# Kernel optimization log

Hardware: AMD Instinct MI355X
Metric: run time of the kernel (lower is better)

## Reference

```python
import jax, jax.numpy as jnp
import numpy as np

# SLAYER neuron / simulation parameters (from network.yaml)
THETA = 10.0      # spike threshold
TAU_SR = 10.0     # SRM (psp) kernel time constant
TAU_REF = 1.0     # refractory kernel time constant
SCALE_REF = 2.0   # refractory scale (kernel = -scaleRef*theta*alpha(t))
TS = 1.0          # simulation step (ms)
TK = 100          # FIR truncation length for the psp kernel (tauSr=10 -> fully decayed)

B, NIN, NHID, NOUT, T = 32, 2312, 512, 10, 350

# discrete refractory kernel ref[n] = C_REF * n * D_REF**n  (alpha shape)
D_REF = float(np.exp(-TS / TAU_REF))
C_REF = float(-SCALE_REF * THETA * np.e * TS / TAU_REF)


def srm_kernel():
    # eps(t) = (t/tauSr) * exp(1 - t/tauSr), peak value 1 at t = tauSr
    t = jnp.arange(TK, dtype=jnp.float32) * TS
    return (t / TAU_SR) * jnp.exp(1.0 - t / TAU_SR)


def psp(x):
    """Causal FIR filter along time. x: [B, C, T] -> [B, C, T]."""
    b, c, t = x.shape
    k = srm_kernel()[::-1].reshape(1, 1, TK)  # lax.conv correlates, so flip
    xp = jnp.pad(x.reshape(b * c, 1, t), ((0, 0), (0, 0), (TK - 1, 0)))
    y = jax.lax.conv_general_dilated(xp, k, (1,), 'VALID')
    return y.reshape(b, c, t)


def dense(W, x):
    # 1x1 conv over channels, applied at every time step
    return jnp.einsum('oi,bit->bot', W, x)


@jax.custom_vjp
def spike_fn(u):
    return (u >= THETA).astype(u.dtype)

def _spike_fwd(u):
    return spike_fn(u), u

def _spike_bwd(u, g):
    # SLAYER surrogate gradient: rho(u) = scaleRho * exp(-|u - theta| / tauRho)
    return (g * jnp.exp(-jnp.abs(u - THETA) / 1.0),)

spike_fn.defvjp(_spike_fwd, _spike_bwd)


def spike_layer(u_in):
    """Threshold-and-refractory spike dynamics via a 2-state IIR realization of
    the alpha refractory kernel. u_in: [B, C, T] -> spikes [B, C, T]."""
    uT = jnp.moveaxis(u_in, -1, 0)  # [T, B, C]
    zero = jnp.zeros(uT.shape[1:], uT.dtype)

    def step(carry, u_t):
        a, b = carry  # a = conv(spikes, D^n), b = conv(spikes, n*D^n)
        u = u_t + C_REF * b          # membrane = psp drive + refractory
        s = spike_fn(u)
        a_new = D_REF * a + s
        b_new = D_REF * b + D_REF * a
        return (a_new, b_new), s

    _, sT = jax.lax.scan(step, (zero, zero), uT)
    return jnp.moveaxis(sT, 0, -1)


def setup_inputs() -> dict:
    key = jax.random.key(0)
    k1, k2, k3 = jax.random.split(key, 3)
    spikeInput = (jax.random.uniform(k1, (B, NIN, T)) < 0.05).astype(jnp.float32)
    W1 = jax.random.normal(k2, (NHID, NIN), dtype=jnp.float32) * 0.05
    W2 = jax.random.normal(k3, (NOUT, NHID), dtype=jnp.float32) * 0.05
    return {"spikeInput": spikeInput, "W1": W1, "W2": W2}


def reference(spikeInput, W1, W2):
    s1 = spike_layer(dense(W1, psp(spikeInput)))
    s2 = spike_layer(dense(W2, psp(s1)))
    return s2
```

## Files before the change

kernel.cpp:

```cpp
#include <hip/hip_runtime.h>
#include <stdint.h>

#define B_SZ   32
#define NIN    2312
#define NHID   512
#define NOUT   10
#define T_SZ   350
#define NW32   73
#define NW64   8
#define NHALF  256
#define NROW   2313

#define DS_D   0.9048374180359595
#define CS_D   0.2718281828459045
#define D100_D 4.5399929762484854e-05
#define DREF_F 0.36787944117144233f
#define CREF_F -54.36563656918091f

#define NCHUNK 7
#define CLEN   50
#define NPF    10

__global__ __launch_bounds__(384) void k12(const float* __restrict__ x,
                                           const float* __restrict__ W1,
                                           uint32_t* __restrict__ bits1,
                                           float* __restrict__ W1s) {
    __shared__ float lds[32 * T_SZ];
    const int bid = blockIdx.x;
    const int tid = threadIdx.x;
    if (bid < NW32 * B_SZ) {
        const int w = bid % NW32;
        const int b = bid / NW32;
        const int rows = (NIN - (w << 5) < 32) ? (NIN - (w << 5)) : 32;
        const float* base = x + ((size_t)(b * NIN + (w << 5))) * T_SZ;
        const int nf4 = (rows * T_SZ) >> 2;
        for (int f = tid; f < nf4; f += 384)
            ((float4*)lds)[f] = ((const float4*)base)[f];
        __syncthreads();
        if (tid < T_SZ) {
            uint32_t bits = 0;
            for (int j = 0; j < rows; ++j)
                bits |= (lds[j * T_SZ + tid] > 0.5f) ? (1u << j) : 0u;
            bits1[(size_t)(b * T_SZ + tid) * NW32 + w] = bits;
        }
    } else if (bid < NW32 * B_SZ + NW32 * 16) {
        float (*tile)[33] = (float (*)[33])lds;
        const int bb = bid - NW32 * B_SZ;
        const int i0 = (bb % NW32) * 32, o0 = (bb / NW32) * 32;
        const int tx = tid & 31, ty = tid >> 5;
#pragma unroll
        for (int r = 0; r < 3; ++r) {
            int row = ty + 12 * r;
            if (row < 32) {
                int o = o0 + row, i = i0 + tx;
                if (i < NIN) tile[row][tx] = W1[(size_t)o * NIN + i];
            }
        }
        __syncthreads();
#pragma unroll
        for (int r = 0; r < 3; ++r) {
            int row = ty + 12 * r;
            if (row < 32) {
                int i = i0 + row, o = o0 + tx;
                if (i < NIN)
                    W1s[((size_t)(o >> 8) * NROW + i) * NHALF + (o & 255)] = tile[tx][row];
            }
        }
    } else {
        if (tid < NHALF) {
            W1s[((size_t)0 * NROW + NIN) * NHALF + tid] = 0.0f;
            W1s[((size_t)1 * NROW + NIN) * NHALF + tid] = 0.0f;
        }
    }
}

__global__ __launch_bounds__(256) void k3_dense1(const uint32_t* __restrict__ bits1,
                                                 const float* __restrict__ W1s,
                                                 float* __restrict__ z1ct) {
    __shared__ uint32_t words[128];
    __shared__ uint16_t pfx[80];
    __shared__ uint16_t idxbuf[NIN + 16];
    __shared__ float red[3][NHALF];
    __shared__ float fin[NHALF];

    const int bt = blockIdx.x;
    const int h = blockIdx.y;
    const int tid = threadIdx.x;
    const int wv = tid >> 6, lane = tid & 63;

    if (tid < 128) words[tid] = (tid < NW32) ? bits1[(size_t)bt * NW32 + tid] : 0u;
    __syncthreads();

    if (wv == 0) {
        uint32_t w0 = words[lane];
        uint32_t w1 = words[lane + 64];
        int p0 = __popc(w0), p1 = __popc(w1);
        int s0 = p0, s1 = p1;
#pragma unroll
        for (int off = 1; off < 64; off <<= 1) {
            int u0 = __shfl_up(s0, off);
            int u1 = __shfl_up(s1, off);
            if (lane >= off) { s0 += u0; s1 += u1; }
        }
        int tot0 = __shfl(s0, 63);
        pfx[lane] = (uint16_t)(s0 - p0);
        if (lane < 9) pfx[lane + 64] = (uint16_t)(tot0 + s1 - p1);
        if (lane == 8) pfx[73] = (uint16_t)(tot0 + s1);
    }
    __syncthreads();

    const int ntot = pfx[73];
    const int npad = (ntot + 15) & ~15;
    if (tid < NW32) {
        uint32_t m = words[tid];
        int p = pfx[tid];
        while (m) {
            int j = __builtin_ctz(m);
            m &= m - 1;
            idxbuf[p++] = (uint16_t)((tid << 5) + j);
        }
    }
    if (tid >= 240) {
        int k = tid - 240;
        if (ntot + k < npad) idxbuf[ntot + k] = (uint16_t)NIN;
    }
    __syncthreads();

    const float* Wh = W1s + (size_t)h * NROW * NHALF;
    float4 acc = make_float4(0.f, 0.f, 0.f, 0.f);
    for (int r = wv; r < npad; r += 16) {
        int i0 = idxbuf[r], i1 = idxbuf[r + 4], i2 = idxbuf[r + 8], i3 = idxbuf[r + 12];
        float4 v0 = ((const float4*)(Wh + (size_t)i0 * NHALF))[lane];
        float4 v1 = ((const float4*)(Wh + (size_t)i1 * NHALF))[lane];
        float4 v2 = ((const float4*)(Wh + (size_t)i2 * NHALF))[lane];
        float4 v3 = ((const float4*)(Wh + (size_t)i3 * NHALF))[lane];
        acc.x += v0.x; acc.y += v0.y; acc.z += v0.z; acc.w += v0.w;
        acc.x += v1.x; acc.y += v1.y; acc.z += v1.z; acc.w += v1.w;
        acc.x += v2.x; acc.y += v2.y; acc.z += v2.z; acc.w += v2.w;
        acc.x += v3.x; acc.y += v3.y; acc.z += v3.z; acc.w += v3.w;
    }
    if (wv > 0) ((float4*)red[wv - 1])[lane] = acc;
    __syncthreads();
    if (wv == 0) {
        float4 a1 = ((float4*)red[0])[lane];
        float4 a2 = ((float4*)red[1])[lane];
        float4 a3 = ((float4*)red[2])[lane];
        acc.x = ((acc.x + a1.x) + a2.x) + a3.x;
        acc.y = ((acc.y + a1.y) + a2.y) + a3.y;
        acc.z = ((acc.z + a1.z) + a2.z) + a3.z;
        acc.w = ((acc.w + a1.w) + a2.w) + a3.w;
        ((float4*)fin)[lane] = acc;
    }
    __syncthreads();
    const int och = (h << 8) + tid;
    const int oc = och >> 6, l6 = och & 63;
    const int b = bt / T_SZ, t = bt - b * T_SZ;
    z1ct[((size_t)(b * NW64 + oc) * T_SZ + t) * 64 + l6] = fin[tid];
}

__global__ __launch_bounds__(512) void k45(const float* __restrict__ z1ct,
                                           const float* __restrict__ W2,
                                           float* __restrict__ z2ct) {
    __shared__ float W2s[NHID * NOUT];
    __shared__ uint64_t sw[CLEN][NW64];
    const int tid = threadIdx.x;
    const int wv = tid >> 6, lane = tid & 63;
    const int b = blockIdx.x / NCHUNK;
    const int ck = blockIdx.x % NCHUNK;
    const int tstart = ck * CLEN;
    const int tend = tstart + CLEN;
    const int t0 = (tstart >= 100) ? tstart - 100 : 0;

    for (int k = tid; k < NHID * NOUT; k += 512) {
        int c = k / NOUT, o = k - c * NOUT;
        W2s[k] = W2[(size_t)o * NHID + c];
    }

    const float* base = z1ct + (size_t)(b * NW64 + wv) * T_SZ * 64 + lane;
    double A = 0.0, Bs = 0.0, A2 = 0.0, Bs2 = 0.0;
    float ra = 0.0f, rb = 0.0f;
    const double TAIL = D100_D * CS_D;
    float xb[NPF], xdb[NPF];
#pragma unroll
    for (int i = 0; i < NPF; ++i) {
        int t = t0 + i;
        xb[i] = base[(size_t)t * 64];
        int td = t - 100;
        xdb[i] = (td >= 0) ? base[(size_t)td * 64] : 0.0f;
    }
    for (int tb = t0; tb < tend; tb += NPF) {
#pragma unroll
        for (int i = 0; i < NPF; ++i) {
            const int t = tb + i;
            float x = xb[i], xd = xdb[i];
            const int tn = t + NPF;
            xb[i] = (tn < T_SZ) ? base[(size_t)tn * 64] : 0.0f;
            const int td = tn - 100;
            xdb[i] = (td >= 0) ? base[(size_t)td * 64] : 0.0f;
            Bs = DS_D * Bs + DS_D * A;
            A = DS_D * A + (double)x;
            Bs2 = DS_D * Bs2 + DS_D * A2;
            A2 = DS_D * A2 + (double)xd;
            double y = CS_D * Bs - TAIL * (Bs2 + 100.0 * A2);
            float u = (float)y + CREF_F * rb;
            float s = (u >= 10.0f) ? 1.0f : 0.0f;
            float ran = DREF_F * ra + s;
            float rbn = DREF_F * rb + DREF_F * ra;
            ra = ran; rb = rbn;
            uint64_t mball = __ballot(s != 0.0f);
            if (t >= tstart && lane == 0) sw[t - tstart][wv] = mball;
        }
    }
    __syncthreads();

    if (tid < CLEN * NOUT) {
        const int tr = tid / NOUT;
        const int o = tid - tr * NOUT;
        const int t = tstart + tr;
        float acc = 0.f;
#pragma unroll
        for (int w2 = 0; w2 < NW64; ++w2) {
            uint64_t m = sw[tr][w2];
            while (m) {
                int j = __builtin_ctzll(m);
                m &= m - 1;
                acc += W2s[((w2 << 6) + j) * NOUT + o];
            }
        }
        const int bo = b * NOUT + o;
        z2ct[((size_t)(bo >> 6) * T_SZ + t) * 64 + (bo & 63)] = acc;
    }
}

__global__ __launch_bounds__(64) void k6_fir_scan2(const float* __restrict__ z2ct,
                                                   float* __restrict__ out) {
    const int lane = threadIdx.x;
    const int g = blockIdx.x / NCHUNK;
    const int ck = blockIdx.x % NCHUNK;
    const int tstart = ck * CLEN;
    const int tend = tstart + CLEN;
    const int t0 = (tstart >= 100) ? tstart - 100 : 0;
    const int bo = (g << 6) + lane;
    const float* base = z2ct + (size_t)g * T_SZ * 64 + lane;
    float* op = out + (size_t)bo * T_SZ;
    double A = 0.0, Bs = 0.0, A2 = 0.0, Bs2 = 0.0;
    float ra = 0.0f, rb = 0.0f;
    const double TAIL = D100_D * CS_D;
    float xb[NPF], xdb[NPF];
#pragma unroll
    for (int i = 0; i < NPF; ++i) {
        int t = t0 + i;
        xb[i] = base[(size_t)t * 64];
        int td = t - 100;
        xdb[i] = (td >= 0) ? base[(size_t)td * 64] : 0.0f;
    }
    for (int tb = t0; tb < tend; tb += NPF) {
#pragma unroll
        for (int i = 0; i < NPF; ++i) {
            const int t = tb + i;
            float x = xb[i], xd = xdb[i];
            const int tn = t + NPF;
            xb[i] = (tn < T_SZ) ? base[(size_t)tn * 64] : 0.0f;
            const int td = tn - 100;
            xdb[i] = (td >= 0) ? base[(size_t)td * 64] : 0.0f;
            Bs = DS_D * Bs + DS_D * A;
            A = DS_D * A + (double)x;
            Bs2 = DS_D * Bs2 + DS_D * A2;
            A2 = DS_D * A2 + (double)xd;
            double y = CS_D * Bs - TAIL * (Bs2 + 100.0 * A2);
            float u = (float)y + CREF_F * rb;
            float s = (u >= 10.0f) ? 1.0f : 0.0f;
            float ran = DREF_F * ra + s;
            float rbn = DREF_F * rb + DREF_F * ra;
            ra = ran; rb = rbn;
            if (t >= tstart) op[t] = s;
        }
    }
}

extern "C" void kernel_launch(void* const* d_in, const int* in_sizes, int n_in,
                              void* d_out, int out_size, void* d_ws, size_t ws_size,
                              hipStream_t stream) {
    const float* spikeInput = (const float*)d_in[0];
    const float* W1 = (const float*)d_in[1];
    const float* W2 = (const float*)d_in[2];
    float* out = (float*)d_out;

    char* ws = (char*)d_ws;
    float* W1s = (float*)(ws + 0);
    uint32_t* bits1 = (uint32_t*)(ws + 4737024);
    float* z1ct = (float*)(ws + 8007424);
    float* z2ct = (float*)(ws + 4737024);

    k12<<<NW32 * B_SZ + NW32 * 16 + 1, 384, 0, stream>>>(spikeInput, W1, bits1, W1s);
    k3_dense1<<<dim3(B_SZ * T_SZ, 2), 256, 0, stream>>>(bits1, W1s, z1ct);
    k45<<<B_SZ * NCHUNK, 512, 0, stream>>>(z1ct, W2, z2ct);
    k6_fir_scan2<<<5 * NCHUNK, 64, 0, stream>>>(z2ct, out);
}
```

Baseline: 316.4 us.

## Batch 32 time-columns per block in sparse dense1 to reuse W1 rows

The sparse dense1 kernel now handles 32 (batch,time) columns per block instead of one. It builds the union of active input rows plus a per-row 32-bit column mask. Each W1 row is then loaded once and added into every column whose mask bit is set, using wave-uniform branches. This is meant to cut repeated global/L2 reads of W1 rows that are shared across columns. In exchange it uses 32 accumulators per thread, more LDS, bit-transpose work, branchy accumulation and a much smaller grid.

Result: slower. 694.8 us (+119.6%).

```diff
diff --git a/kernel.cpp b/kernel.cpp
--- a/kernel.cpp
+++ b/kernel.cpp
@@ -20,6 +20,9 @@
 #define NCHUNK 7
 #define CLEN   50
 #define NPF    10
+
+#define GCOL   32
+#define NGRP   350
 
 __global__ __launch_bounds__(384) void k12(const float* __restrict__ x,
                                            const float* __restrict__ W1,
@@ -77,23 +80,45 @@
 __global__ __launch_bounds__(256) void k3_dense1(const uint32_t* __restrict__ bits1,
                                                  const float* __restrict__ W1s,
                                                  float* __restrict__ z1ct) {
-    __shared__ uint32_t words[128];
+    __shared__ uint32_t colw[GCOL * NW32];
+    __shared__ uint32_t orw[128];
+    __shared__ uint32_t rowmask[GCOL * NW32];
     __shared__ uint16_t pfx[80];
-    __shared__ uint16_t idxbuf[NIN + 16];
-    __shared__ float red[3][NHALF];
-    __shared__ float fin[NHALF];
-
-    const int bt = blockIdx.x;
+    __shared__ uint16_t idxbuf[NIN + 8];
+    __shared__ float red[GCOL][NHALF];
+
+    const int bt0 = blockIdx.x * GCOL;
     const int h = blockIdx.y;
     const int tid = threadIdx.x;
-    const int wv = tid >> 6, lane = tid & 63;
-
-    if (tid < 128) words[tid] = (tid < NW32) ? bits1[(size_t)bt * NW32 + tid] : 0u;
+    const int lane = tid & 63;
+    const int wv = tid >> 6;
+    const int g = tid >> 7;
+    const int l = tid & 127;
+
+    const uint32_t* bsrc = bits1 + (size_t)bt0 * NW32;
+    if (tid < 128) orw[tid] = 0;
+    for (int k = tid; k < GCOL * NW32; k += 256) colw[k] = bsrc[k];
+    __syncthreads();
+
+    if (tid < NW32) {
+        uint32_t o = 0;
+#pragma unroll
+        for (int c = 0; c < GCOL; ++c) o |= colw[c * NW32 + tid];
+        orw[tid] = o;
+    }
+    for (int k = tid; k < GCOL * NW32; k += 256) {
+        const int w = k >> 5, j = k & 31;
+        uint32_t m = 0;
+#pragma unroll
+        for (int c = 0; c < GCOL; ++c)
+            m |= ((colw[c * NW32 + w] >> j) & 1u) << c;
+        rowmask[k] = m;
+    }
     __syncthreads();
 
     if (wv == 0) {
-        uint32_t w0 = words[lane];
-        uint32_t w1 = words[lane + 64];
+        uint32_t w0 = orw[lane];
+        uint32_t w1 = orw[lane + 64];
         int p0 = __popc(w0), p1 = __popc(w1);
         int s0 = p0, s1 = p1;
 #pragma unroll
@@ -108,11 +133,10 @@
         if (lane == 8) pfx[73] = (uint16_t)(tot0 + s1);
     }
     __syncthreads();
-
     const int ntot = pfx[73];
-    const int npad = (ntot + 15) & ~15;
+    const int npad = (ntot + 7) & ~7;
     if (tid < NW32) {
-        uint32_t m = words[tid];
+        uint32_t m = orw[tid];
         int p = pfx[tid];
         while (m) {
             int j = __builtin_ctz(m);
@@ -120,42 +144,75 @@
             idxbuf[p++] = (uint16_t)((tid << 5) + j);
         }
     }
-    if (tid >= 240) {
-        int k = tid - 240;
+    if (tid >= 248) {
+        int k = tid - 248;
         if (ntot + k < npad) idxbuf[ntot + k] = (uint16_t)NIN;
     }
     __syncthreads();
 
     const float* Wh = W1s + (size_t)h * NROW * NHALF;
-    float4 acc = make_float4(0.f, 0.f, 0.f, 0.f);
-    for (int r = wv; r < npad; r += 16) {
-        int i0 = idxbuf[r], i1 = idxbuf[r + 4], i2 = idxbuf[r + 8], i3 = idxbuf[r + 12];
-        float4 v0 = ((const float4*)(Wh + (size_t)i0 * NHALF))[lane];
-        float4 v1 = ((const float4*)(Wh + (size_t)i1 * NHALF))[lane];
-        float4 v2 = ((const float4*)(Wh + (size_t)i2 * NHALF))[lane];
-        float4 v3 = ((const float4*)(Wh + (size_t)i3 * NHALF))[lane];
-        acc.x += v0.x; acc.y += v0.y; acc.z += v0.z; acc.w += v0.w;
-        acc.x += v1.x; acc.y += v1.y; acc.z += v1.z; acc.w += v1.w;
-        acc.x += v2.x; acc.y += v2.y; acc.z += v2.z; acc.w += v2.w;
-        acc.x += v3.x; acc.y += v3.y; acc.z += v3.z; acc.w += v3.w;
-    }
-    if (wv > 0) ((float4*)red[wv - 1])[lane] = acc;
-    __syncthreads();
-    if (wv == 0) {
-        float4 a1 = ((float4*)red[0])[lane];
-        float4 a2 = ((float4*)red[1])[lane];
-        float4 a3 = ((float4*)red[2])[lane];
-        acc.x = ((acc.x + a1.x) + a2.x) + a3.x;
-        acc.y = ((acc.y + a1.y) + a2.y) + a3.y;
-        acc.z = ((acc.z + a1.z) + a2.z) + a3.z;
-        acc.w = ((acc.w + a1.w) + a2.w) + a3.w;
-        ((float4*)fin)[lane] = acc;
+    float2 acc[GCOL];
+#pragma unroll
+    for (int c = 0; c < GCOL; ++c) acc[c] = make_float2(0.f, 0.f);
+
+#define PROCROW(MM, VV)                                                     \
+    {                                                                       \
+        uint32_t mu = __builtin_amdgcn_readfirstlane((int)(MM));            \
+        _Pragma("unroll")                                                   \
+        for (int q = 0; q < 4; ++q) {                                       \
+            if (mu & (0xFFu << (q * 8))) {                                  \
+                _Pragma("unroll")                                           \
+                for (int c8 = 0; c8 < 8; ++c8) {                            \
+                    const int c = q * 8 + c8;                               \
+                    if (mu & (1u << c)) {                                   \
+                        acc[c].x += (VV).x;                                 \
+                        acc[c].y += (VV).y;                                 \
+                    }                                                       \
+                }                                                           \
+            }                                                               \
+        }                                                                   \
+    }
+
+    for (int r = g; r < npad; r += 8) {
+        const int i0 = idxbuf[r],     i1 = idxbuf[r + 2];
+        const int i2 = idxbuf[r + 4], i3 = idxbuf[r + 6];
+        const uint32_t m0 = rowmask[i0], m1 = rowmask[i1];
+        const uint32_t m2 = rowmask[i2], m3 = rowmask[i3];
+        const float2 v0 = *(const float2*)(Wh + (size_t)i0 * NHALF + 2 * l);
+        const float2 v1 = *(const float2*)(Wh + (size_t)i1 * NHALF + 2 * l);
+        const float2 v2 = *(const float2*)(Wh + (size_t)i2 * NHALF + 2 * l);
+        const float2 v3 = *(const float2*)(Wh + (size_t)i3 * NHALF + 2 * l);
+        PROCROW(m0, v0)
+        PROCROW(m1, v1)
+        PROCROW(m2, v2)
+        PROCROW(m3, v3)
+    }
+#undef PROCROW
+
+    if (g == 1) {
+#pragma unroll
+        for (int c = 0; c < GCOL; ++c)
+            *(float2*)&red[c][2 * l] = acc[c];
+    }
+    __syncthreads();
+    if (g == 0) {
+#pragma unroll
+        for (int c = 0; c < GCOL; ++c) {
+            float2 o = *(float2*)&red[c][2 * l];
+            o.x += acc[c].x;
+            o.y += acc[c].y;
+            *(float2*)&red[c][2 * l] = o;
+        }
     }
     __syncthreads();
     const int och = (h << 8) + tid;
     const int oc = och >> 6, l6 = och & 63;
-    const int b = bt / T_SZ, t = bt - b * T_SZ;
-    z1ct[((size_t)(b * NW64 + oc) * T_SZ + t) * 64 + l6] = fin[tid];
+#pragma unroll
+    for (int c = 0; c < GCOL; ++c) {
+        const int bt = bt0 + c;
+        const int b = bt / T_SZ, t = bt - b * T_SZ;
+        z1ct[((size_t)(b * NW64 + oc) * T_SZ + t) * 64 + l6] = red[c][tid];
+    }
 }
 
 __global__ __launch_bounds__(512) void k45(const float* __restrict__ z1ct,
@@ -293,7 +350,7 @@
     float* z2ct = (float*)(ws + 4737024);
 
     k12<<<NW32 * B_SZ + NW32 * 16 + 1, 384, 0, stream>>>(spikeInput, W1, bits1, W1s);
-    k3_dense1<<<dim3(B_SZ * T_SZ, 2), 256, 0, stream>>>(bits1, W1s, z1ct);
+    k3_dense1<<<dim3(NGRP, 2), 256, 0, stream>>>(bits1, W1s, z1ct);
     k45<<<B_SZ * NCHUNK, 512, 0, stream>>>(z1ct, W2, z2ct);
     k6_fir_scan2<<<5 * NCHUNK, 64, 0, stream>>>(z2ct, out);
 }
```
